# Optimization experiments

Measured on AMD Instinct MI355X. Metric: run time of the kernel, lower is better.

The kernel has to match this reference:

```python
import jax, jax.numpy as jnp
import numpy as np

B, N, T, D, DG, DS, NC = 16, 64, 256, 64, 64, 9, 2

def _pe(times, d, max_len):
    # PositionalEncodingTF: timescales = max_len ** linspace(0,1,d//2)
    ts = jnp.asarray(max_len ** np.linspace(0.0, 1.0, d // 2), jnp.float32)
    st = times[..., None] / ts
    return jnp.concatenate([jnp.sin(st), jnp.cos(st)], -1)

def _ln(h, g, b):
    m = h.mean(-1, keepdims=True)
    v = ((h - m) ** 2).mean(-1, keepdims=True)
    return (h - m) * jax.lax.rsqrt(v + 1e-5) * g + b

def setup_inputs():
    key = jax.random.key(0)
    ks = jax.random.split(key, 40)
    s = 0.02
    value = jax.random.normal(ks[0], (B, T, N))
    obs = (jax.random.uniform(ks[1], (B, T, N)) < 0.5).astype(jnp.float32)
    times = jnp.sort(jax.random.uniform(ks[2], (B, T)) * T, axis=1)
    F = D + 2 * DG  # per-node GRU input feature size [x_t, h, time_enc]
    return dict(
        x=jnp.concatenate([value, obs, times[..., None]], -1),
        nufft=jax.random.normal(ks[3], (B, 2, T, N)),
        delta_t=jax.random.uniform(ks[4], (B, T)) * 0.1,
        static=jax.random.normal(ks[5], (B, DS)),
        lengths=jax.random.randint(ks[6], (B,), 1, T + 1),
        proj_w=jax.random.normal(ks[7], (2, D)) * s, proj_b=jnp.zeros(D),
        Wqkv=jax.random.normal(ks[8], (D, 3 * D)) * s, bqkv=jnp.zeros(3 * D),
        Wo=jax.random.normal(ks[9], (D, D)) * s, bo=jnp.zeros(D),
        ln1_g=jnp.ones(D), ln1_b=jnp.zeros(D),
        W1=jax.random.normal(ks[10], (D, D)) * s, b1=jnp.zeros(D),
        W2=jax.random.normal(ks[11], (D, D)) * s, b2=jnp.zeros(D),
        ln2_g=jnp.ones(D), ln2_b=jnp.zeros(D),
        WQ_f=jax.random.normal(ks[12], (T, T)) * 0.05,
        WK_f=jax.random.normal(ks[13], (T, T)) * 0.05,
        Wz=jax.random.normal(ks[14], (2 * F, DG)) * s, bz=jnp.zeros(DG),
        Wr=jax.random.normal(ks[15], (2 * F, DG)) * s, br=jnp.zeros(DG),
        Wc=jax.random.normal(ks[16], (2 * F, DG)) * s, bc=jnp.zeros(DG),
        Wfin=jax.random.normal(ks[17], (DG,)) * s, bfin=jnp.zeros(()),
        We=jax.random.normal(ks[18], (DS, N)) * s, be=jnp.zeros(N),
        Wc1=jax.random.normal(ks[19], (2 * N, 200)) * s, bc1=jnp.zeros(200),
        Wc2=jax.random.normal(ks[20], (200, NC)) * s, bc2=jnp.zeros(NC),
    )

def _forward(x, nufft, delta_t, static, lengths, proj_w, proj_b, Wqkv, bqkv, Wo, bo,
             ln1_g, ln1_b, W1, b1, W2, b2, ln2_g, ln2_b, WQ_f, WK_f,
             Wz, bz, Wr, br, Wc, bc, Wfin, bfin, We, be, Wc1, bc1, Wc2, bc2):
    lengths = jnp.maximum(lengths, 1)
    value = x[:, :, :N].transpose(0, 2, 1)          # (B,N,T)
    obs = x[:, :, N:2 * N].transpose(0, 2, 1)       # (B,N,T) observation mask
    times = x[:, :, -1]                              # (B,T)
    # Conv2d(2->D, 1x1) input projection == per-element linear over [value, mask]
    feat = jnp.stack([value, obs], -1) @ proj_w + proj_b   # (B,N,T,D)
    pe1 = _pe(times, D, T)                           # (B,T,D)
    tin = feat + pe1[:, None]                        # (B,N,T,D)
    # single-head transformer encoder layer (post-norm, relu FFN, eval: no dropout)
    qkv = tin @ Wqkv + bqkv
    q, k, v = jnp.split(qkv, 3, -1)
    scores = jnp.einsum('bnqd,bnkd->bnqk', q, k) / jnp.sqrt(jnp.float32(D))
    kpad = jnp.arange(T)[None, :] >= lengths[:, None]      # (B,T) key padding
    scores = jnp.where(kpad[:, None, None, :], -1e9, scores)
    attn = jax.nn.softmax(scores, -1)
    ao = jnp.einsum('bnqk,bnkd->bnqd', attn, v) @ Wo + bo
    h1 = _ln(tin + ao, ln1_g, ln1_b)
    ff = jax.nn.relu(h1 @ W1 + b1) @ W2 + b2
    tout = _ln(h1 + ff, ln2_g, ln2_b)
    m = obs[..., None]
    x_tat = m * tin + (1.0 - m) * tout               # masked blend (B,N,T,D)
    # Variable_Attention_layer on nufft channel 1: relu-score softmax attention
    xf = nufft[:, 1].transpose(0, 2, 1)              # (B,N,T)
    S = jax.nn.relu(jnp.einsum('bnt,bmt->bnm', xf @ WQ_f, xf @ WK_f)) / jnp.sqrt(jnp.float32(T))
    A = jax.nn.softmax(S, -1).mean(0)                # (N,N)
    A = 0.5 * (A + A.T)
    sm = jax.nn.softmax(A, -1)
    A = 0.5 * (sm + sm.T)
    pe2 = _pe(times, DG, T)                          # (B,T,DG)
    # graph-conv GRU over time (CGRNN) with delta_t decay + length masking
    def stepf(h, inputs):
        xt, tet, dtt, t = inputs                     # (B,N,D),(B,DG),(B,),()
        h = h * jnp.exp(-jax.nn.relu(dtt))[:, None, None]
        te = jnp.broadcast_to(tet[:, None, :], (h.shape[0], N, DG))
        inp = jnp.concatenate([xt, h, te], -1)
        gin = jnp.concatenate([inp, jnp.einsum('nm,bmf->bnf', A, inp)], -1)
        z = jax.nn.sigmoid(gin @ Wz + bz)
        r = jax.nn.sigmoid(gin @ Wr + br)
        inc = jnp.concatenate([xt, r * h, te], -1)
        cin = jnp.concatenate([inc, jnp.einsum('nm,bmf->bnf', A, inc)], -1)
        c = jnp.tanh(cin @ Wc + bc)
        hn = z * h + (1.0 - z) * c
        h = jnp.where((t < lengths)[:, None, None], hn, h)
        return h, None
    h0 = jnp.zeros((x.shape[0], N, DG), x.dtype)
    xs = (x_tat.transpose(2, 0, 1, 3), pe2.transpose(1, 0, 2), delta_t.T, jnp.arange(T))
    hT, _ = jax.lax.scan(stepf, h0, xs)
    out = hT @ Wfin + bfin                           # final 1x1 conv -> (B,N)
    emb = static @ We + be                           # (B,N)
    hcl = jax.nn.relu(jnp.concatenate([out, emb], -1) @ Wc1 + bc1)
    return hcl @ Wc2 + bc2                           # (B,NC)

def reference(x, nufft, delta_t, static, lengths, proj_w, proj_b, Wqkv, bqkv, Wo, bo,
              ln1_g, ln1_b, W1, b1, W2, b2, ln2_g, ln2_b, WQ_f, WK_f,
              Wz, bz, Wr, br, Wc, bc, Wfin, bfin, We, be, Wc1, bc1, Wc2, bc2):
    return _forward(x, nufft, delta_t, static, lengths, proj_w, proj_b, Wqkv, bqkv, Wo, bo,
                    ln1_g, ln1_b, W1, b1, W2, b2, ln2_g, ln2_b, WQ_f, WK_f,
                    Wz, bz, Wr, br, Wc, bc, Wfin, bfin, We, be, Wc1, bc1, Wc2, bc2)
```

## Files before the change

### kernel.cpp

```cpp
#include <hip/hip_runtime.h>
#include <hip/hip_bf16.h>
#include <cmath>

#define DEV __device__ __forceinline__

typedef short s16x8 __attribute__((ext_vector_type(8)));
typedef short s16x4 __attribute__((ext_vector_type(4)));
typedef float f32x4 __attribute__((ext_vector_type(4)));
typedef int   i32x2 __attribute__((ext_vector_type(2)));

DEV unsigned short f2bu(float x){
  __hip_bfloat16 h = __float2bfloat16(x);
  return *reinterpret_cast<unsigned short*>(&h);
}
DEV float bs2f(unsigned short v){ return __uint_as_float(((unsigned)v)<<16); }
DEV float bs2f(short v){ return bs2f((unsigned short)v); }

DEV unsigned cvtpk(float lo, float hi){
  unsigned r;
  asm("v_cvt_pk_bf16_f32 %0, %1, %2" : "=v"(r) : "v"(lo), "v"(hi));
  return r;
}
DEV float dppx1(float v){
  int r = __builtin_amdgcn_mov_dpp(__float_as_int(v), 0xB1, 0xF, 0xF, true);
  return __int_as_float(r);
}

#define BAR() do { asm volatile("s_waitcnt lgkmcnt(0)" ::: "memory"); \
                   __builtin_amdgcn_s_barrier(); \
                   __builtin_amdgcn_sched_barrier(0); } while(0)

DEV int swzo(int row, int col){
  return (row*128 + ((col*2) ^ ((row&7)<<4))) >> 1;
}
DEV s16x8 ldfrag(const short* tile, int t16, int lane, int kk){
  int row = t16 + (lane & 15);
  int c0  = (kk<<5) + ((lane>>4)<<3);
  int off = (row*128 + ((c0<<1) ^ ((row&7)<<4))) >> 1;
  return *(const s16x8*)(tile + off);
}
DEV int swzv(int d, int t){
  return (d*512 + ((t*2) ^ ((d&7)<<4))) >> 1;
}

__global__ void k0_prep(const float* __restrict__ Wqkv, const float* __restrict__ Wo,
                        const float* __restrict__ W1, const float* __restrict__ W2,
                        const float* __restrict__ Wz, const float* __restrict__ Wr,
                        const float* __restrict__ Wc,
                        short* __restrict__ Wqkv_t, short* __restrict__ Wo_t,
                        short* __restrict__ W1_t, short* __restrict__ W2_t,
                        short* __restrict__ Wg_t, short* __restrict__ Wg_h)
{
  int t = blockIdx.x*256 + threadIdx.x;
  if (t < 12288){ int nn=t>>6, k=t&63; Wqkv_t[t]=(short)f2bu(Wqkv[k*192+nn]); }
  else if (t < 16384){ int e=t-12288; int nn=e>>6,k=e&63; Wo_t[e]=(short)f2bu(Wo[k*64+nn]); }
  else if (t < 20480){ int e=t-16384; int nn=e>>6,k=e&63; W1_t[e]=(short)f2bu(W1[k*64+nn]); }
  else if (t < 24576){ int e=t-20480; int nn=e>>6,k=e&63; W2_t[e]=(short)f2bu(W2[k*64+nn]); }
  else if (t < 49152){
    int e=t-24576;
    int g=e>>13, rem=e&8191, s=rem>>12, rem2=rem&4095, c=rem2>>6, k=rem2&63;
    const float* Wg = (g==0)?Wz:((g==1)?Wr:Wc);
    Wg_t[e] = (short)f2bu(Wg[((s?192:0)+k)*64 + c]);
  }
  else if (t < 73728){
    int e=t-49152;
    int g=e>>13, rem=e&8191, s=rem>>12, rem2=rem&4095, c=rem2>>6, k=rem2&63;
    const float* Wg = (g==0)?Wz:((g==1)?Wr:Wc);
    Wg_h[e] = (short)f2bu(Wg[((s?256:64)+k)*64 + c]);
  }
}

__global__ void k1_pe_u(const float* __restrict__ x, const float* __restrict__ delta_t,
                        const float* __restrict__ Wz, const float* __restrict__ bz,
                        const float* __restrict__ Wr, const float* __restrict__ br,
                        const float* __restrict__ Wc, const float* __restrict__ bc,
                        float* __restrict__ pe, float* __restrict__ U, float* __restrict__ decay)
{
  const int bt = blockIdx.x;
  const int d  = threadIdx.x;
  __shared__ float pes[64];
  float tmv = x[(size_t)bt*129 + 128];
  int j = d & 31;
  float ts = exp2f((float)j * (8.0f/31.0f));
  float st = tmv / ts;
  float v = (d < 32) ? sinf(st) : cosf(st);
  pes[d] = v;
  pe[(size_t)bt*64 + d] = v;
  __syncthreads();
  float a0=bz[d], a1=0.f, a2=br[d], a3=0.f, a4=bc[d], a5=0.f;
  for (int k=0;k<64;k++){
    float p = pes[k];
    a0 = fmaf(p, Wz[(128+k)*64+d], a0);
    a1 = fmaf(p, Wz[(320+k)*64+d], a1);
    a2 = fmaf(p, Wr[(128+k)*64+d], a2);
    a3 = fmaf(p, Wr[(320+k)*64+d], a3);
    a4 = fmaf(p, Wc[(128+k)*64+d], a4);
    a5 = fmaf(p, Wc[(320+k)*64+d], a5);
  }
  float* u = U + (size_t)bt*384;
  u[d]=a0; u[64+d]=a1; u[128+d]=a2; u[192+d]=a3; u[256+d]=a4; u[320+d]=a5;
  if (d==0) decay[bt] = expf(-fmaxf(delta_t[bt], 0.f));
}

__global__ void k2a_qfkf(const float* __restrict__ nufft, const float* __restrict__ WQf,
                         const float* __restrict__ WKf, float* __restrict__ qf, float* __restrict__ kf)
{
  const int bn = blockIdx.x, b = bn>>6, n = bn&63;
  const int u = threadIdx.x;
  __shared__ float xs[256];
  xs[u] = nufft[ ((((size_t)b*2)+1)*256 + u)*64 + n ];
  __syncthreads();
  float aq=0.f, ak=0.f;
  for (int t=0;t<256;t++){
    float xv = xs[t];
    aq = fmaf(xv, WQf[t*256+u], aq);
    ak = fmaf(xv, WKf[t*256+u], ak);
  }
  qf[(size_t)bn*256+u]=aq;
  kf[(size_t)bn*256+u]=ak;
}

__launch_bounds__(256, 1)
__global__ void k2b_soft(const float* __restrict__ qf, const float* __restrict__ kf,
                         float* __restrict__ soft)
{
  const int b = blockIdx.x, tid = threadIdx.x;
  __shared__ float qs[64*257];
  __shared__ float ksh[64*257];
  __shared__ float Ss[64*65];
  const float* qb = qf + ((size_t)b<<14);
  const float* kb = kf + ((size_t)b<<14);
  for (int e=tid; e<16384; e+=256){
    int r=e>>8, c=e&255;
    qs[r*257+c]=qb[e];
    ksh[r*257+c]=kb[e];
  }
  __syncthreads();
  const int n = tid>>2, m0 = (tid&3)<<4;
  float acc[16];
  #pragma unroll
  for (int i=0;i<16;i++) acc[i]=0.f;
  for (int t=0;t<256;t++){
    float qv = qs[n*257+t];
    #pragma unroll
    for (int i=0;i<16;i++) acc[i] = fmaf(qv, ksh[(m0+i)*257+t], acc[i]);
  }
  #pragma unroll
  for (int i=0;i<16;i++) Ss[n*65+m0+i] = fmaxf(acc[i],0.f)*(1.f/16.f);
  __syncthreads();
  if (tid < 64){
    float mx=-1e30f;
    for (int m=0;m<64;m++) mx=fmaxf(mx, Ss[tid*65+m]);
    float s=0.f;
    for (int m=0;m<64;m++) s += expf(Ss[tid*65+m]-mx);
    float inv=1.f/s;
    for (int m=0;m<64;m++) soft[((size_t)b<<12)+(tid<<6)+m] = expf(Ss[tid*65+m]-mx)*inv;
  }
}

__global__ void k2c_A(const float* __restrict__ soft, short* __restrict__ Abf,
                      float* __restrict__ rs_out)
{
  const int tid = threadIdx.x;
  __shared__ float A0[64*65];
  __shared__ float A1[64*65];
  for (int e=tid; e<4096; e+=256){
    int nn=e>>6, mm=e&63;
    float s=0.f;
    #pragma unroll
    for (int b=0;b<16;b++) s += soft[((size_t)b<<12)+e];
    A0[nn*65+mm] = s*(1.f/16.f);
  }
  __syncthreads();
  for (int e=tid; e<4096; e+=256){
    int nn=e>>6, mm=e&63;
    A1[nn*65+mm] = 0.5f*(A0[nn*65+mm]+A0[mm*65+nn]);
  }
  __syncthreads();
// ... 247 lines not shown
      const int rb=(rt<<4)+(lhi<<2);
      #pragma unroll
      for (int dt=0;dt<4;dt++){
        const int col=(dt<<4)+l15;
        const short* wb = W1_t + (col<<6)+(lhi<<3);
        s16x8 b0=*(const s16x8*)wb, b1v=*(const s16x8*)(wb+32);
        float bias=b1[col];
        f32x4 acc={bias,bias,bias,bias};
        acc=__builtin_amdgcn_mfma_f32_16x16x32_bf16(a0,b0,acc,0,0,0);
        acc=__builtin_amdgcn_mfma_f32_16x16x32_bf16(a1,b1v,acc,0,0,0);
        #pragma unroll
        for(int i=0;i<4;i++) tp_s[swzo(rb+i,col)]=(short)f2bu(fmaxf(acc[i],0.f));
      }
    }
  }
  __syncthreads();

  #pragma unroll
  for (int j=0;j<2;j++){
    const int rt=w+(j<<3);
    if (rt < LT){
      s16x8 a0=ldfrag(tp_s, rt<<4, lane, 0);
      s16x8 a1=ldfrag(tp_s, rt<<4, lane, 1);
      const int rb=(rt<<4)+(lhi<<2);
      f32x4 to[4];
      #pragma unroll
      for (int dt=0;dt<4;dt++){
        const int col=(dt<<4)+l15;
        const short* wb = W2_t + (col<<6)+(lhi<<3);
        s16x8 b0=*(const s16x8*)wb, b1v=*(const s16x8*)(wb+32);
        float bias=b2[col];
        f32x4 acc={bias,bias,bias,bias};
        acc=__builtin_amdgcn_mfma_f32_16x16x32_bf16(a0,b0,acc,0,0,0);
        acc=__builtin_amdgcn_mfma_f32_16x16x32_bf16(a1,b1v,acc,0,0,0);
        acc += h1[j][dt];
        to[dt]=acc;
      }
      f32x4 mu, rsq;
      #pragma unroll
      for(int i=0;i<4;i++){
        float sv = to[0][i]+to[1][i]+to[2][i]+to[3][i];
        sv += __shfl_xor(sv,1); sv+=__shfl_xor(sv,2); sv+=__shfl_xor(sv,4); sv+=__shfl_xor(sv,8);
        mu[i]=sv*(1.f/64.f);
      }
      #pragma unroll
      for(int i=0;i<4;i++){
        float sv=0.f;
        #pragma unroll
        for(int dt=0;dt<4;dt++){ float c=to[dt][i]-mu[i]; sv=fmaf(c,c,sv); }
        sv += __shfl_xor(sv,1); sv+=__shfl_xor(sv,2); sv+=__shfl_xor(sv,4); sv+=__shfl_xor(sv,8);
        rsq[i]=1.f/sqrtf(sv*(1.f/64.f)+1e-5f);
      }
      #pragma unroll
      for(int dt=0;dt<4;dt++){
        const int col=(dt<<4)+l15;
        float g=ln2g[col], bb=ln2b[col];
        #pragma unroll
        for(int i=0;i<4;i++){
          const int row=rb+i;
          if (row < len){
            float tv=(to[dt][i]-mu[i])*rsq[i]*g+bb;
            float tin = fmaf(valr[row],proj_w[col], fmaf(obsr[row],proj_w[64+col], proj_b[col]))
                      + pe_g[(((size_t)b<<8)+row)*64+col];
            float ob = obsr[row];
            xtat[((size_t)bn<<14)+(row<<6)+col] = f2bu(ob*tin + (1.f-ob)*tv);
          }
        }
      }
    }
  }
}

__global__ void k35_xg(const unsigned short* __restrict__ xtat, const short* __restrict__ Abf,
                       const short* __restrict__ Wg_t, const int* __restrict__ lengths,
                       const float* __restrict__ U, const float* __restrict__ rs_g,
                       unsigned short* __restrict__ Xall)
{
  const int bt = blockIdx.x, b = bt>>8, t = bt&255;
  int len = lengths[b]; if (len<1) len=1;
  if (t >= len) return;
  const int tid = threadIdx.x, w = tid>>6, lane = tid&63;
  const int l15 = lane&15, lhi = lane>>4;
  __shared__ short xt_rm[4096], xt_tp[4096], axt_rm[4096];

  #pragma unroll
  for (int q=0;q<2;q++){
    int e = tid + (q<<8);
    int nn = e>>3, c0 = (e&7)<<3;
    s16x8 v = *(const s16x8*)((const short*)xtat + (((size_t)(b*64+nn)*256 + t)<<6) + c0);
    *(s16x8*)(xt_rm + swzo(nn,c0)) = v;
    #pragma unroll
    for (int jj=0;jj<8;jj++) xt_tp[swzo(c0+jj, nn)] = v[jj];
  }
  __syncthreads();

  {
    s16x8 bx[2];
    #pragma unroll
    for (int kk=0;kk<2;kk++) bx[kk]=ldfrag(xt_tp, w<<4, lane, kk);
    #pragma unroll
    for (int rt=0;rt<4;rt++){
      f32x4 acc={0.f,0.f,0.f,0.f};
      #pragma unroll
      for (int kk=0;kk<2;kk++){
        s16x8 af = *(const s16x8*)(Abf + ((rt<<4)+l15)*64 + (kk<<5) + (lhi<<3));
        acc=__builtin_amdgcn_mfma_f32_16x16x32_bf16(af,bx[kk],acc,0,0,0);
      }
      const int rb=(rt<<4)+(lhi<<2);
      #pragma unroll
      for(int i=0;i<4;i++) axt_rm[swzo(rb+i,(w<<4)+l15)] = (short)f2bu(acc[i]);
    }
  }
  __syncthreads();

  s16x8 fx[4][2], fa[4][2];
  #pragma unroll
  for (int rt=0;rt<4;rt++)
    #pragma unroll
    for (int kk=0;kk<2;kk++){
      fx[rt][kk]=ldfrag(xt_rm, rt<<4, lane, kk);
      fa[rt][kk]=ldfrag(axt_rm, rt<<4, lane, kk);
    }
  const int dcol = (w<<4)+l15;
  f32x4 rsv[4];
  #pragma unroll
  for (int rt=0;rt<4;rt++) rsv[rt] = *(const f32x4*)(rs_g + (rt<<4) + (lhi<<2));
  const float* Ub = U + (size_t)bt*384;
  #pragma unroll
  for (int g=0; g<3; g++){
    s16x8 wbx[2], wba[2];
    #pragma unroll
    for (int kk=0;kk<2;kk++){
      wbx[kk] = *(const s16x8*)(Wg_t + (((g<<1)  )*64 + dcol)*64 + (kk<<5)+(lhi<<3));
      wba[kk] = *(const s16x8*)(Wg_t + (((g<<1)+1)*64 + dcol)*64 + (kk<<5)+(lhi<<3));
    }
    float u1 = Ub[(g<<7) + dcol];
    float u2 = Ub[(g<<7) + 64 + dcol];
    #pragma unroll
    for (int rt=0;rt<4;rt++){
      f32x4 acc={u1,u1,u1,u1};
      #pragma unroll
      for (int kk=0;kk<2;kk++){
        acc=__builtin_amdgcn_mfma_f32_16x16x32_bf16(fx[rt][kk],wbx[kk],acc,0,0,0);
        acc=__builtin_amdgcn_mfma_f32_16x16x32_bf16(fa[rt][kk],wba[kk],acc,0,0,0);
      }
      s16x4 pk;
      #pragma unroll
      for(int i=0;i<4;i++) pk[i]=(short)f2bu(acc[i] + rsv[rt][i]*u2);
      *(s16x4*)((short*)Xall + (((size_t)bt*3 + g)*64 + dcol)*64 + (rt<<4)+(lhi<<2)) = pk;
    }
  }
}

__launch_bounds__(512, 1)
__global__ void k4_scan(const unsigned short* __restrict__ Xall,
                        const float* __restrict__ decay, const short* __restrict__ Abf,
                        const short* __restrict__ Wg_h,
                        const int* __restrict__ lengths, float* __restrict__ hT)
{
  const int b = blockIdx.x, tid = threadIdx.x;
  const int w = tid>>6, lane = tid&63;
  const int l15 = lane&15, lhi = lane>>4;
  const int pe_ = l15&1;
  const int rnt = w>>1, dp = w&1;
  const int nb_ = (rnt<<4) + (lhi<<2);
  const int d0 = (dp<<5) + l15, d1 = (dp<<5) + 16 + l15;
  const int tmA0 = (w&1)<<1, tmA1 = tmA0+1;
  const int dnA = w>>1;

  __shared__ short h_rm[4096], h_tp[4096], ah_rm[4096];
  __shared__ short rh_rm[4096], rh_tp[4096], arh_rm[4096];
  __shared__ float dec_s[256];

  int len = lengths[b]; if (len<1) len=1;
  for (int e=tid; e<256; e+=512) dec_s[e] = decay[b*256+e];

  s16x8 aA[2][2];
  #pragma unroll
  for (int t2=0;t2<2;t2++)
    #pragma unroll
    for (int kk=0;kk<2;kk++)
      aA[t2][kk] = *(const s16x8*)(Abf + (((t2?tmA1:tmA0)<<4) + l15)*64 + (kk<<5) + (lhi<<3));

  s16x8 wf[3][2][2][2];
  #pragma unroll
  for (int g=0;g<3;g++)
    #pragma unroll
    for (int s=0;s<2;s++)
      #pragma unroll
      for (int kk=0;kk<2;kk++)
        #pragma unroll
        for (int e=0;e<2;e++)
          wf[g][s][kk][e] = *(const s16x8*)(Wg_h + (((g*2+s)*64 + (e?d1:d0))<<6) + (kk<<5) + (lhi<<3));

  int tpo[2];
  #pragma unroll
  for (int e=0;e<2;e++){ int r = e?d1:d0; tpo[e] = r*128 + (((nb_)*2) ^ ((r&7)<<4)); }
  int rmo[4];
  { int dPr = ((dp<<1) + pe_)*16 + (l15 & ~1);
    #pragma unroll
    for (int i=0;i<4;i++){ int n = nb_+i; rmo[i] = n*128 + ((dPr*2) ^ ((n&7)<<4)); } }
  int amo[4];
  { int dAr = (dnA<<4) + (l15 & ~1);
    int tb = (pe_? tmA1 : tmA0)<<4;
    #pragma unroll
    for (int i=0;i<4;i++){ int n = tb + (lhi<<2) + i; amo[i] = n*128 + ((dAr*2) ^ ((n&7)<<4)); } }
  int rdT[2], rdR[2];
  { int r = (dnA<<4)+l15;
    #pragma unroll
    for (int kk=0;kk<2;kk++) rdT[kk] = r*128 + (((kk<<6) + (lhi<<4)) ^ ((r&7)<<4)); }
  { int r = (rnt<<4)+l15;
    #pragma unroll
    for (int kk=0;kk<2;kk++) rdR[kk] = r*128 + (((kk<<6) + (lhi<<4)) ^ ((r&7)<<4)); }

  f32x4 hreg[2] = {{0.f,0.f,0.f,0.f},{0.f,0.f,0.f,0.f}};
  f32x4 zz[2];

  const short* Xb = (const short*)Xall;
  s16x4 xzc[2], xrc[2], xcc[2], xzn[2], xrn[2], xcn[2];
  #pragma unroll
  for (int e=0;e<2;e++){ xzc[e]=(s16x4){0,0,0,0}; xrc[e]=xzc[e]; xcc[e]=xzc[e]; }
  {
    const short* base = Xb + ((size_t)(b*256))*12288;
    #pragma unroll
    for (int e=0;e<2;e++){
      int de = e?d1:d0;
      xzc[e] = *(const s16x4*)(base + (0*64 + de)*64 + nb_);
      xrc[e] = *(const s16x4*)(base + (1*64 + de)*64 + nb_);
      xcc[e] = *(const s16x4*)(base + (2*64 + de)*64 + nb_);
    }
  }
  __syncthreads();

  for (int t=0; t<len; t++){
    float dc = dec_s[t];
    #pragma unroll
    for (int e=0;e<2;e++)
      #pragma unroll
      for (int i=0;i<4;i++) hreg[e][i] *= dc;

    #pragma unroll
    for (int e=0;e<2;e++){ xzn[e]=(s16x4){0,0,0,0}; xrn[e]=xzn[e]; xcn[e]=xzn[e]; }
    if (t+1 < len){
      const short* base = Xb + ((size_t)(b*256 + t+1))*12288;
      #pragma unroll
      for (int e=0;e<2;e++){
        int de = e?d1:d0;
        xzn[e] = *(const s16x4*)(base + (0*64 + de)*64 + nb_);
        xrn[e] = *(const s16x4*)(base + (1*64 + de)*64 + nb_);
        xcn[e] = *(const s16x4*)(base + (2*64 + de)*64 + nb_);
      }
    }

    #pragma unroll
    for (int e=0;e<2;e++){
      i32x2 v; v[0] = (int)cvtpk(hreg[e][0], hreg[e][1]);
               v[1] = (int)cvtpk(hreg[e][2], hreg[e][3]);
      *(i32x2*)((char*)h_tp + tpo[e]) = v;
    }
    #pragma unroll
    for (int i=0;i<4;i++){
      float v0 = hreg[0][i], v1 = hreg[1][i];
      float n0 = dppx1(v0), n1 = dppx1(v1);
      float lo = pe_ ? n1 : v0;
      float hi = pe_ ? v1 : n0;
      *(unsigned*)((char*)h_rm + rmo[i]) = cvtpk(lo, hi);
    }
    BAR();

    {
      s16x8 bh0 = *(const s16x8*)((const char*)h_tp + rdT[0]);
      s16x8 bh1 = *(const s16x8*)((const char*)h_tp + rdT[1]);
      f32x4 a0v={0.f,0.f,0.f,0.f}, a1v={0.f,0.f,0.f,0.f};
      a0v = __builtin_amdgcn_mfma_f32_16x16x32_bf16(aA[0][0], bh0, a0v, 0,0,0);
      a0v = __builtin_amdgcn_mfma_f32_16x16x32_bf16(aA[0][1], bh1, a0v, 0,0,0);
      a1v = __builtin_amdgcn_mfma_f32_16x16x32_bf16(aA[1][0], bh0, a1v, 0,0,0);
      a1v = __builtin_amdgcn_mfma_f32_16x16x32_bf16(aA[1][1], bh1, a1v, 0,0,0);
      #pragma unroll
      for (int i=0;i<4;i++){
        float n0 = dppx1(a0v[i]), n1 = dppx1(a1v[i]);
        float lo = pe_ ? n1 : a0v[i];
        float hi = pe_ ? a1v[i] : n0;
        *(unsigned*)((char*)ah_rm + amo[i]) = cvtpk(lo, hi);
      }
    }
    BAR();

    {
      s16x8 fh0 = *(const s16x8*)((const char*)h_rm  + rdR[0]);
      s16x8 fh1 = *(const s16x8*)((const char*)h_rm  + rdR[1]);
      s16x8 fa0 = *(const s16x8*)((const char*)ah_rm + rdR[0]);
      s16x8 fa1 = *(const s16x8*)((const char*)ah_rm + rdR[1]);
      f32x4 gz[2], gr[2], rh[2];
      #pragma unroll
      for (int e=0;e<2;e++)
        #pragma unroll
        for (int i=0;i<4;i++){ gz[e][i]=bs2f(xzc[e][i]); gr[e][i]=bs2f(xrc[e][i]); }
      #pragma unroll
      for (int e=0;e<2;e++){
        gz[e] = __builtin_amdgcn_mfma_f32_16x16x32_bf16(fh0, wf[0][0][0][e], gz[e], 0,0,0);
        gz[e] = __builtin_amdgcn_mfma_f32_16x16x32_bf16(fh1, wf[0][0][1][e], gz[e], 0,0,0);
        gz[e] = __builtin_amdgcn_mfma_f32_16x16x32_bf16(fa0, wf[0][1][0][e], gz[e], 0,0,0);
        gz[e] = __builtin_amdgcn_mfma_f32_16x16x32_bf16(fa1, wf[0][1][1][e], gz[e], 0,0,0);
        gr[e] = __builtin_amdgcn_mfma_f32_16x16x32_bf16(fh0, wf[1][0][0][e], gr[e], 0,0,0);
        gr[e] = __builtin_amdgcn_mfma_f32_16x16x32_bf16(fh1, wf[1][0][1][e], gr[e], 0,0,0);
        gr[e] = __builtin_amdgcn_mfma_f32_16x16x32_bf16(fa0, wf[1][1][0][e], gr[e], 0,0,0);
        gr[e] = __builtin_amdgcn_mfma_f32_16x16x32_bf16(fa1, wf[1][1][1][e], gr[e], 0,0,0);
      }
      #pragma unroll
      for (int e=0;e<2;e++)
        #pragma unroll
        for (int i=0;i<4;i++){
          float zv = 1.f/(1.f+__expf(-gz[e][i]));
          float rv = 1.f/(1.f+__expf(-gr[e][i]));
          zz[e][i] = zv;
          rh[e][i] = rv * hreg[e][i];
        }
      #pragma unroll
      for (int e=0;e<2;e++){
        i32x2 v; v[0] = (int)cvtpk(rh[e][0], rh[e][1]);
                 v[1] = (int)cvtpk(rh[e][2], rh[e][3]);
        *(i32x2*)((char*)rh_tp + tpo[e]) = v;
      }
      #pragma unroll
      for (int i=0;i<4;i++){
        float v0 = rh[0][i], v1 = rh[1][i];
        float n0 = dppx1(v0), n1 = dppx1(v1);
        float lo = pe_ ? n1 : v0;
        float hi = pe_ ? v1 : n0;
        *(unsigned*)((char*)rh_rm + rmo[i]) = cvtpk(lo, hi);
      }
    }
    BAR();

    {
      s16x8 br0 = *(const s16x8*)((const char*)rh_tp + rdT[0]);
      s16x8 br1 = *(const s16x8*)((const char*)rh_tp + rdT[1]);
      f32x4 a0v={0.f,0.f,0.f,0.f}, a1v={0.f,0.f,0.f,0.f};
      a0v = __builtin_amdgcn_mfma_f32_16x16x32_bf16(aA[0][0], br0, a0v, 0,0,0);
      a0v = __builtin_amdgcn_mfma_f32_16x16x32_bf16(aA[0][1], br1, a0v, 0,0,0);
      a1v = __builtin_amdgcn_mfma_f32_16x16x32_bf16(aA[1][0], br0, a1v, 0,0,0);
      a1v = __builtin_amdgcn_mfma_f32_16x16x32_bf16(aA[1][1], br1, a1v, 0,0,0);
      #pragma unroll
      for (int i=0;i<4;i++){
        float n0 = dppx1(a0v[i]), n1 = dppx1(a1v[i]);
        float lo = pe_ ? n1 : a0v[i];
        float hi = pe_ ? a1v[i] : n0;
        *(unsigned*)((char*)arh_rm + amo[i]) = cvtpk(lo, hi);
      }
    }
    BAR();

    {
      s16x8 fr0 = *(const s16x8*)((const char*)rh_rm  + rdR[0]);
      s16x8 fr1 = *(const s16x8*)((const char*)rh_rm  + rdR[1]);
      s16x8 fb0 = *(const s16x8*)((const char*)arh_rm + rdR[0]);
      s16x8 fb1 = *(const s16x8*)((const char*)arh_rm + rdR[1]);
      f32x4 gc[2];
      #pragma unroll
      for (int e=0;e<2;e++)
        #pragma unroll
        for (int i=0;i<4;i++) gc[e][i]=bs2f(xcc[e][i]);
      #pragma unroll
      for (int e=0;e<2;e++){
        gc[e] = __builtin_amdgcn_mfma_f32_16x16x32_bf16(fr0, wf[2][0][0][e], gc[e], 0,0,0);
        gc[e] = __builtin_amdgcn_mfma_f32_16x16x32_bf16(fr1, wf[2][0][1][e], gc[e], 0,0,0);
        gc[e] = __builtin_amdgcn_mfma_f32_16x16x32_bf16(fb0, wf[2][1][0][e], gc[e], 0,0,0);
        gc[e] = __builtin_amdgcn_mfma_f32_16x16x32_bf16(fb1, wf[2][1][1][e], gc[e], 0,0,0);
      }
      #pragma unroll
      for (int e=0;e<2;e++)
        #pragma unroll
        for (int i=0;i<4;i++){
          float cv = 1.f - 2.f/(__expf(2.f*gc[e][i])+1.f);
          hreg[e][i] = fmaf(zz[e][i], hreg[e][i]-cv, cv);
        }
    }

    #pragma unroll
    for (int e=0;e<2;e++){ xzc[e]=xzn[e]; xrc[e]=xrn[e]; xcc[e]=xcn[e]; }
  }

  float sp = 1.f;
  for (int t=len; t<256; t++) sp *= dec_s[t];
  #pragma unroll
  for (int e=0;e<2;e++)
    #pragma unroll
    for (int i=0;i<4;i++)
      hT[(((size_t)b<<6) + nb_ + i)*64 + (e?d1:d0)] = hreg[e][i]*sp;
}

__global__ void k5_head(const float* __restrict__ hT, const float* __restrict__ Wfin,
                        const float* __restrict__ bfin,
                        const float* __restrict__ stat, const float* __restrict__ We,
                        const float* __restrict__ be,
                        const float* __restrict__ Wc1, const float* __restrict__ bc1,
                        const float* __restrict__ Wc2, const float* __restrict__ bc2,
                        float* __restrict__ out)
{
  const int b = blockIdx.x, tid = threadIdx.x;
  __shared__ float cat[128];
  __shared__ float hcl[200];
  if (tid < 64){
    const float* hr = hT + (((size_t)b<<6)+tid)*64;
    float a = bfin[0];
    #pragma unroll
    for (int d=0;d<64;d++) a = fmaf(hr[d], Wfin[d], a);
    cat[tid]=a;
  } else if (tid < 128){
    int nn = tid-64;
    float a = be[nn];
    #pragma unroll
    for (int k=0;k<9;k++) a = fmaf(stat[b*9+k], We[k*64+nn], a);
    cat[tid]=a;
  }
  __syncthreads();
  if (tid < 200){
    float a = bc1[tid];
    for (int k=0;k<128;k++) a = fmaf(cat[k], Wc1[k*200+tid], a);
    hcl[tid] = fmaxf(a, 0.f);
  }
  __syncthreads();
  if (tid < 2){
    float a = bc2[tid];
    for (int k=0;k<200;k++) a = fmaf(hcl[k], Wc2[k*2+tid], a);
    out[b*2+tid] = a;
  }
}

extern "C" void kernel_launch(void* const* d_in, const int* in_sizes, int n_in,
                              void* d_out, int out_size, void* d_ws, size_t ws_size,
                              hipStream_t stream)
{
  const float* x       = (const float*)d_in[0];
  const float* nufft   = (const float*)d_in[1];
  const float* delta_t = (const float*)d_in[2];
  const float* stat    = (const float*)d_in[3];
  const int*   lengths = (const int*)  d_in[4];
  const float* proj_w  = (const float*)d_in[5];
  const float* proj_b  = (const float*)d_in[6];
  const float* Wqkv    = (const float*)d_in[7];
  const float* bqkv    = (const float*)d_in[8];
  const float* Wo      = (const float*)d_in[9];
  const float* bo      = (const float*)d_in[10];
  const float* ln1g    = (const float*)d_in[11];
  const float* ln1b    = (const float*)d_in[12];
  const float* W1      = (const float*)d_in[13];
  const float* b1      = (const float*)d_in[14];
  const float* W2      = (const float*)d_in[15];
  const float* b2      = (const float*)d_in[16];
  const float* ln2g    = (const float*)d_in[17];
  const float* ln2b    = (const float*)d_in[18];
  const float* WQf     = (const float*)d_in[19];
  const float* WKf     = (const float*)d_in[20];
  const float* Wz      = (const float*)d_in[21];
  const float* bz      = (const float*)d_in[22];
  const float* Wr      = (const float*)d_in[23];
  const float* br      = (const float*)d_in[24];
  const float* Wc      = (const float*)d_in[25];
  const float* bc      = (const float*)d_in[26];
  const float* Wfin    = (const float*)d_in[27];
  const float* bfin    = (const float*)d_in[28];
  const float* We      = (const float*)d_in[29];
  const float* be      = (const float*)d_in[30];
  const float* Wc1     = (const float*)d_in[31];
  const float* bc1     = (const float*)d_in[32];
  const float* Wc2     = (const float*)d_in[33];
  const float* bc2     = (const float*)d_in[34];
  float* out = (float*)d_out;

  char* ws = (char*)d_ws;
  size_t o = 0;
  float* pe    = (float*)(ws+o); o += (size_t)4096*64*4;
  float* U     = (float*)(ws+o); o += (size_t)4096*384*4;
  float* decay = (float*)(ws+o); o += (size_t)4096*4;
  unsigned short* xtat = (unsigned short*)(ws+o); o += (size_t)1024*256*64*2;
  float* qf    = (float*)(ws+o); o += (size_t)1024*256*4;
  float* kf    = (float*)(ws+o); o += (size_t)1024*256*4;
  float* soft  = (float*)(ws+o); o += (size_t)16*4096*4;
  short* Abf   = (short*)(ws+o); o += (size_t)4096*2;
  float* rs    = (float*)(ws+o); o += (size_t)64*4;
  float* hT    = (float*)(ws+o); o += (size_t)16*64*64*4;
  short* Wqkv_t= (short*)(ws+o); o += (size_t)12288*2;
  short* Wo_t  = (short*)(ws+o); o += (size_t)4096*2;
  short* W1_t  = (short*)(ws+o); o += (size_t)4096*2;
  short* W2_t  = (short*)(ws+o); o += (size_t)4096*2;
  short* Wg_t  = (short*)(ws+o); o += (size_t)24576*2;
  short* Wg_h  = (short*)(ws+o); o += (size_t)24576*2;
  unsigned short* Xall = (unsigned short*)(ws+o); o += (size_t)4096*3*4096*2;
  (void)ws_size; (void)in_sizes; (void)n_in; (void)out_size;

  hipLaunchKernelGGL(k0_prep,   dim3(288),  dim3(256), 0, stream,
                     Wqkv, Wo, W1, W2, Wz, Wr, Wc, Wqkv_t, Wo_t, W1_t, W2_t, Wg_t, Wg_h);
  hipLaunchKernelGGL(k1_pe_u,   dim3(4096), dim3(64),  0, stream,
                     x, delta_t, Wz, bz, Wr, br, Wc, bc, pe, U, decay);
  hipLaunchKernelGGL(k2a_qfkf,  dim3(1024), dim3(256), 0, stream,
                     nufft, WQf, WKf, qf, kf);
  hipLaunchKernelGGL(k2b_soft,  dim3(16),   dim3(256), 0, stream, qf, kf, soft);
  hipLaunchKernelGGL(k2c_A,     dim3(1),    dim3(256), 0, stream, soft, Abf, rs);
  hipLaunchKernelGGL(k3_former, dim3(1024), dim3(512), 0, stream,
                     x, pe, proj_w, proj_b, Wqkv_t, bqkv, Wo_t, bo, ln1g, ln1b,
                     W1_t, b1, W2_t, b2, ln2g, ln2b, lengths, xtat);
  hipLaunchKernelGGL(k35_xg,    dim3(4096), dim3(256), 0, stream,
                     xtat, Abf, Wg_t, lengths, U, rs, Xall);
  hipLaunchKernelGGL(k4_scan,   dim3(16),   dim3(512), 0, stream,
                     Xall, decay, Abf, Wg_h, lengths, hT);
  hipLaunchKernelGGL(k5_head,   dim3(16),   dim3(256), 0, stream,
                     hT, Wfin, bfin, stat, We, be, Wc1, bc1, Wc2, bc2, out);
}
```

Baseline: 864.9 us.

## Reassociate graph mixing after weight projection in GRU scan, cut barriers to two

The recurrent scan now computes (h·W_a) first and then applies the adjacency A to that product (A·(hW) instead of (A·h)·W). Each wave owns 16 output features for all 64 nodes, so the separate A·h and A·(r*h) stages and their shared-memory buffers go away. Each timestep now needs two barriers instead of four. The block shrinks from 512 to 256 threads, and the decay multiply moves to the end of the step. In exchange, each wave does more MFMA work per step, the intermediate is rounded to bf16 at a different point, and register pressure is higher.

```diff
diff --git a/kernel.cpp b/kernel.cpp
--- a/kernel.cpp
+++ b/kernel.cpp
@@ -24,6 +24,16 @@
 DEV float dppx1(float v){
   int r = __builtin_amdgcn_mov_dpp(__float_as_int(v), 0xB1, 0xF, 0xF, true);
   return __int_as_float(r);
+}
+DEV f32x4 mfma16(s16x4 a, s16x4 b, f32x4 c){
+  asm("v_mfma_f32_16x16x16_bf16 %0, %1, %2, %0" : "+v"(c) : "v"(a), "v"(b));
+  return c;
+}
+DEV s16x4 packbf(f32x4 v){
+  union { i32x2 u; s16x4 s; } r;
+  r.u[0] = (int)cvtpk(v[0], v[1]);
+  r.u[1] = (int)cvtpk(v[2], v[3]);
+  return r.s;
 }
 
 #define BAR() do { asm volatile("s_waitcnt lgkmcnt(0)" ::: "memory"); \
@@ -577,7 +587,7 @@
   }
 }
 
-__launch_bounds__(512, 1)
+__launch_bounds__(256, 1)
 __global__ void k4_scan(const unsigned short* __restrict__ Xall,
                         const float* __restrict__ decay, const short* __restrict__ Abf,
                         const short* __restrict__ Wg_h,
@@ -585,234 +595,221 @@
 {
   const int b = blockIdx.x, tid = threadIdx.x;
   const int w = tid>>6, lane = tid&63;
-  const int l15 = lane&15, lhi = lane>>4;
-  const int pe_ = l15&1;
-  const int rnt = w>>1, dp = w&1;
-  const int nb_ = (rnt<<4) + (lhi<<2);
-  const int d0 = (dp<<5) + l15, d1 = (dp<<5) + 16 + l15;
-  const int tmA0 = (w&1)<<1, tmA1 = tmA0+1;
-  const int dnA = w>>1;
-
-  __shared__ short h_rm[4096], h_tp[4096], ah_rm[4096];
-  __shared__ short rh_rm[4096], rh_tp[4096], arh_rm[4096];
+  const int l15 = lane&15, g = lane>>4;
+  const int pe = l15&1;
+  const int dg = (w<<4) + l15;
+
+  __shared__ short h_rm[4096];
+  __shared__ short rh_rm[4096];
   __shared__ float dec_s[256];
 
   int len = lengths[b]; if (len<1) len=1;
-  for (int e=tid; e<256; e+=512) dec_s[e] = decay[b*256+e];
-
-  s16x8 aA[2][2];
-  #pragma unroll
-  for (int t2=0;t2<2;t2++)
-    #pragma unroll
-    for (int kk=0;kk<2;kk++)
-      aA[t2][kk] = *(const s16x8*)(Abf + (((t2?tmA1:tmA0)<<4) + l15)*64 + (kk<<5) + (lhi<<3));
-
-  s16x8 wf[3][2][2][2];
-  #pragma unroll
-  for (int g=0;g<3;g++)
+  dec_s[tid] = decay[b*256+tid];
+
+  s16x4 aA[4][4];
+  #pragma unroll
+  for (int nt=0;nt<4;nt++)
+    #pragma unroll
+    for (int kc=0;kc<4;kc++)
+      aA[nt][kc] = *(const s16x4*)(Abf + ((nt<<4)+l15)*64 + (kc<<4) + (g<<2));
+
+  s16x8 wfB[3][2][2];
+  #pragma unroll
+  for (int g3=0;g3<3;g3++)
     #pragma unroll
     for (int s=0;s<2;s++)
       #pragma unroll
-      for (int kk=0;kk<2;kk++)
-        #pragma unroll
-        for (int e=0;e<2;e++)
-          wf[g][s][kk][e] = *(const s16x8*)(Wg_h + (((g*2+s)*64 + (e?d1:d0))<<6) + (kk<<5) + (lhi<<3));
-
-  int tpo[2];
-  #pragma unroll
-  for (int e=0;e<2;e++){ int r = e?d1:d0; tpo[e] = r*128 + (((nb_)*2) ^ ((r&7)<<4)); }
-  int rmo[4];
-  { int dPr = ((dp<<1) + pe_)*16 + (l15 & ~1);
-    #pragma unroll
-    for (int i=0;i<4;i++){ int n = nb_+i; rmo[i] = n*128 + ((dPr*2) ^ ((n&7)<<4)); } }
-  int amo[4];
-  { int dAr = (dnA<<4) + (l15 & ~1);
-    int tb = (pe_? tmA1 : tmA0)<<4;
-    #pragma unroll
-    for (int i=0;i<4;i++){ int n = tb + (lhi<<2) + i; amo[i] = n*128 + ((dAr*2) ^ ((n&7)<<4)); } }
-  int rdT[2], rdR[2];
-  { int r = (dnA<<4)+l15;
-    #pragma unroll
-    for (int kk=0;kk<2;kk++) rdT[kk] = r*128 + (((kk<<6) + (lhi<<4)) ^ ((r&7)<<4)); }
-  { int r = (rnt<<4)+l15;
-    #pragma unroll
-    for (int kk=0;kk<2;kk++) rdR[kk] = r*128 + (((kk<<6) + (lhi<<4)) ^ ((r&7)<<4)); }
-
-  f32x4 hreg[2] = {{0.f,0.f,0.f,0.f},{0.f,0.f,0.f,0.f}};
-  f32x4 zz[2];
-
-  const short* Xb = (const short*)Xall;
-  s16x4 xzc[2], xrc[2], xcc[2], xzn[2], xrn[2], xcn[2];
-  #pragma unroll
-  for (int e=0;e<2;e++){ xzc[e]=(s16x4){0,0,0,0}; xrc[e]=xzc[e]; xcc[e]=xzc[e]; }
+      for (int kc=0;kc<2;kc++)
+        wfB[g3][s][kc] = *(const s16x8*)(Wg_h + (((g3*2+s)*64 + dg)<<6) + (kc<<5) + (g<<3));
+
   {
-    const short* base = Xb + ((size_t)(b*256))*12288;
-    #pragma unroll
-    for (int e=0;e<2;e++){
-      int de = e?d1:d0;
-      xzc[e] = *(const s16x4*)(base + (0*64 + de)*64 + nb_);
-      xrc[e] = *(const s16x4*)(base + (1*64 + de)*64 + nb_);
-      xcc[e] = *(const s16x4*)(base + (2*64 + de)*64 + nb_);
-    }
-  }
+    s16x8 z8 = {0,0,0,0,0,0,0,0};
+    *(s16x8*)(h_rm + tid*16) = z8;
+    *(s16x8*)(h_rm + tid*16 + 8) = z8;
+  }
+
+  int rdo[4][2];
+  #pragma unroll
+  for (int nt=0;nt<4;nt++)
+    #pragma unroll
+    for (int kc=0;kc<2;kc++){
+      int r = (nt<<4) + l15;
+      rdo[nt][kc] = r*128 + (((kc<<6) + (g<<4)) ^ ((r&7)<<4));
+    }
+  int wro[4][2];
+  {
+    int pb = (w<<5) + ((l15&~1)<<1);
+    #pragma unroll
+    for (int nt=0;nt<4;nt++)
+      #pragma unroll
+      for (int q=0;q<2;q++){
+        int i = (pe<<1) + q;
+        int nrow = (nt<<4) + (g<<2) + i;
+        wro[nt][q] = nrow*128 + (pb ^ ((nrow&7)<<4));
+      }
+  }
+
+  f32x4 hreg[4] = {{0,0,0,0},{0,0,0,0},{0,0,0,0},{0,0,0,0}};
+  f32x4 zz[4];
+
+  const unsigned short* Xbase = Xall + ((size_t)(b*256))*12288;
+  int xoff[3][4];
+  #pragma unroll
+  for (int g3=0;g3<3;g3++)
+    #pragma unroll
+    for (int nt=0;nt<4;nt++)
+      xoff[g3][nt] = ((g3<<6) + dg)*64 + (nt<<4) + (g<<2);
+
+  s16x4 xc[3][4], xn[3][4];
+  #pragma unroll
+  for (int g3=0;g3<3;g3++)
+    #pragma unroll
+    for (int nt=0;nt<4;nt++)
+      xc[g3][nt] = *(const s16x4*)(Xbase + xoff[g3][nt]);
+
   __syncthreads();
 
   for (int t=0; t<len; t++){
-    float dc = dec_s[t];
-    #pragma unroll
-    for (int e=0;e<2;e++)
-      #pragma unroll
-      for (int i=0;i<4;i++) hreg[e][i] *= dc;
-
-    #pragma unroll
-    for (int e=0;e<2;e++){ xzn[e]=(s16x4){0,0,0,0}; xrn[e]=xzn[e]; xcn[e]=xzn[e]; }
     if (t+1 < len){
-      const short* base = Xb + ((size_t)(b*256 + t+1))*12288;
-      #pragma unroll
-      for (int e=0;e<2;e++){
-        int de = e?d1:d0;
-        xzn[e] = *(const s16x4*)(base + (0*64 + de)*64 + nb_);
-        xrn[e] = *(const s16x4*)(base + (1*64 + de)*64 + nb_);
-        xcn[e] = *(const s16x4*)(base + (2*64 + de)*64 + nb_);
-      }
-    }
-
-    #pragma unroll
-    for (int e=0;e<2;e++){
-      i32x2 v; v[0] = (int)cvtpk(hreg[e][0], hreg[e][1]);
-               v[1] = (int)cvtpk(hreg[e][2], hreg[e][3]);
-      *(i32x2*)((char*)h_tp + tpo[e]) = v;
-    }
+      const unsigned short* bp = Xbase + (size_t)(t+1)*12288;
+      #pragma unroll
+      for (int g3=0;g3<3;g3++)
+        #pragma unroll
+        for (int nt=0;nt<4;nt++)
+          xn[g3][nt] = *(const s16x4*)(bp + xoff[g3][nt]);
+    } else {
+      #pragma unroll
+      for (int g3=0;g3<3;g3++)
+        #pragma unroll
+        for (int nt=0;nt<4;nt++)
+          xn[g3][nt] = (s16x4){0,0,0,0};
+    }
+
+    s16x8 hf[4][2];
+    #pragma unroll
+    for (int nt=0;nt<4;nt++)
+      #pragma unroll
+      for (int kc=0;kc<2;kc++)
+        hf[nt][kc] = *(const s16x8*)((const char*)h_rm + rdo[nt][kc]);
+
+    f32x4 gz[4], gr[4], yz[4], yr[4];
+    #pragma unroll
+    for (int nt=0;nt<4;nt++){
+      #pragma unroll
+      for (int i=0;i<4;i++){
+        gz[nt][i] = bs2f(xc[0][nt][i]);
+        gr[nt][i] = bs2f(xc[1][nt][i]);
+      }
+      yz[nt] = (f32x4){0,0,0,0};
+      yr[nt] = (f32x4){0,0,0,0};
+    }
+    #pragma unroll
+    for (int nt=0;nt<4;nt++)
+      #pragma unroll
+      for (int kc=0;kc<2;kc++){
+        gz[nt] = __builtin_amdgcn_mfma_f32_16x16x32_bf16(hf[nt][kc], wfB[0][0][kc], gz[nt], 0,0,0);
+        yz[nt] = __builtin_amdgcn_mfma_f32_16x16x32_bf16(hf[nt][kc], wfB[0][1][kc], yz[nt], 0,0,0);
+        gr[nt] = __builtin_amdgcn_mfma_f32_16x16x32_bf16(hf[nt][kc], wfB[1][0][kc], gr[nt], 0,0,0);
+        yr[nt] = __builtin_amdgcn_mfma_f32_16x16x32_bf16(hf[nt][kc], wfB[1][1][kc], yr[nt], 0,0,0);
+      }
+    s16x4 yzp[4], yrp[4];
+    #pragma unroll
+    for (int nt=0;nt<4;nt++){ yzp[nt]=packbf(yz[nt]); yrp[nt]=packbf(yr[nt]); }
+    #pragma unroll
+    for (int nt=0;nt<4;nt++)
+      #pragma unroll
+      for (int kc=0;kc<4;kc++){
+        gz[nt] = mfma16(aA[nt][kc], yzp[kc], gz[nt]);
+        gr[nt] = mfma16(aA[nt][kc], yrp[kc], gr[nt]);
+      }
+    f32x4 rh[4];
+    #pragma unroll
+    for (int nt=0;nt<4;nt++)
+      #pragma unroll
+      for (int i=0;i<4;i++){
+        float zv = __builtin_amdgcn_rcpf(1.f + __expf(-gz[nt][i]));
+        float rv = __builtin_amdgcn_rcpf(1.f + __expf(-gr[nt][i]));
+        zz[nt][i] = zv;
+        rh[nt][i] = rv * hreg[nt][i];
+      }
+    #pragma unroll
+    for (int nt=0;nt<4;nt++)
+      #pragma unroll
+      for (int q=0;q<2;q++){
+        int i = (pe<<1) + q;
+        float v = rh[nt][i];
+        float nv = dppx1(v);
+        unsigned word = pe ? cvtpk(nv, v) : cvtpk(v, nv);
+        *(unsigned*)((char*)rh_rm + wro[nt][q]) = word;
+      }
+    BAR();
+
+    s16x8 rf[4][2];
+    #pragma unroll
+    for (int nt=0;nt<4;nt++)
+      #pragma unroll
+      for (int kc=0;kc<2;kc++)
+        rf[nt][kc] = *(const s16x8*)((const char*)rh_rm + rdo[nt][kc]);
+
+    f32x4 gc[4], yc[4];
+    #pragma unroll
+    for (int nt=0;nt<4;nt++){
+      #pragma unroll
+      for (int i=0;i<4;i++) gc[nt][i] = bs2f(xc[2][nt][i]);
+      yc[nt] = (f32x4){0,0,0,0};
+    }
+    #pragma unroll
+    for (int nt=0;nt<4;nt++)
+      #pragma unroll
+      for (int kc=0;kc<2;kc++){
+        gc[nt] = __builtin_amdgcn_mfma_f32_16x16x32_bf16(rf[nt][kc], wfB[2][0][kc], gc[nt], 0,0,0);
+        yc[nt] = __builtin_amdgcn_mfma_f32_16x16x32_bf16(rf[nt][kc], wfB[2][1][kc], yc[nt], 0,0,0);
+      }
+    s16x4 ycp[4];
+    #pragma unroll
+    for (int nt=0;nt<4;nt++) ycp[nt]=packbf(yc[nt]);
+    #pragma unroll
+    for (int nt=0;nt<4;nt++)
+      #pragma unroll
+      for (int kc=0;kc<4;kc++)
+        gc[nt] = mfma16(aA[nt][kc], ycp[kc], gc[nt]);
+
+    float dcn = (t+1 < len) ? dec_s[t+1] : 1.f;
+    #pragma unroll
+    for (int nt=0;nt<4;nt++)
+      #pragma unroll
+      for (int i=0;i<4;i++){
+        float cv = 1.f - 2.f*__builtin_amdgcn_rcpf(__expf(2.f*gc[nt][i]) + 1.f);
+        float hn = cv + zz[nt][i]*(hreg[nt][i] - cv);
+        hreg[nt][i] = hn * dcn;
+      }
+    #pragma unroll
+    for (int nt=0;nt<4;nt++)
+      #pragma unroll
+      for (int q=0;q<2;q++){
+        int i = (pe<<1) + q;
+        float v = hreg[nt][i];
+        float nv = dppx1(v);
+        unsigned word = pe ? cvtpk(nv, v) : cvtpk(v, nv);
+        *(unsigned*)((char*)h_rm + wro[nt][q]) = word;
+      }
+    #pragma unroll
+    for (int g3=0;g3<3;g3++)
+      #pragma unroll
+      for (int nt=0;nt<4;nt++)
+        xc[g3][nt] = xn[g3][nt];
+    BAR();
+  }
+
+  float sp = 1.f;
+  for (int t2=len; t2<256; t2++) sp *= dec_s[t2];
+  #pragma unroll
+  for (int nt=0;nt<4;nt++)
     #pragma unroll
     for (int i=0;i<4;i++){
-      float v0 = hreg[0][i], v1 = hreg[1][i];
-      float n0 = dppx1(v0), n1 = dppx1(v1);
-      float lo = pe_ ? n1 : v0;
-      float hi = pe_ ? v1 : n0;
-      *(unsigned*)((char*)h_rm + rmo[i]) = cvtpk(lo, hi);
-    }
-    BAR();
-
-    {
-      s16x8 bh0 = *(const s16x8*)((const char*)h_tp + rdT[0]);
-      s16x8 bh1 = *(const s16x8*)((const char*)h_tp + rdT[1]);
-      f32x4 a0v={0.f,0.f,0.f,0.f}, a1v={0.f,0.f,0.f,0.f};
-      a0v = __builtin_amdgcn_mfma_f32_16x16x32_bf16(aA[0][0], bh0, a0v, 0,0,0);
-      a0v = __builtin_amdgcn_mfma_f32_16x16x32_bf16(aA[0][1], bh1, a0v, 0,0,0);
-      a1v = __builtin_amdgcn_mfma_f32_16x16x32_bf16(aA[1][0], bh0, a1v, 0,0,0);
-      a1v = __builtin_amdgcn_mfma_f32_16x16x32_bf16(aA[1][1], bh1, a1v, 0,0,0);
-      #pragma unroll
-      for (int i=0;i<4;i++){
-        float n0 = dppx1(a0v[i]), n1 = dppx1(a1v[i]);
-        float lo = pe_ ? n1 : a0v[i];
-        float hi = pe_ ? a1v[i] : n0;
-        *(unsigned*)((char*)ah_rm + amo[i]) = cvtpk(lo, hi);
-      }
-    }
-    BAR();
-
-    {
-      s16x8 fh0 = *(const s16x8*)((const char*)h_rm  + rdR[0]);
-      s16x8 fh1 = *(const s16x8*)((const char*)h_rm  + rdR[1]);
-      s16x8 fa0 = *(const s16x8*)((const char*)ah_rm + rdR[0]);
-      s16x8 fa1 = *(const s16x8*)((const char*)ah_rm + rdR[1]);
-      f32x4 gz[2], gr[2], rh[2];
-      #pragma unroll
-      for (int e=0;e<2;e++)
-        #pragma unroll
-        for (int i=0;i<4;i++){ gz[e][i]=bs2f(xzc[e][i]); gr[e][i]=bs2f(xrc[e][i]); }
-      #pragma unroll
-      for (int e=0;e<2;e++){
-        gz[e] = __builtin_amdgcn_mfma_f32_16x16x32_bf16(fh0, wf[0][0][0][e], gz[e], 0,0,0);
-        gz[e] = __builtin_amdgcn_mfma_f32_16x16x32_bf16(fh1, wf[0][0][1][e], gz[e], 0,0,0);
-        gz[e] = __builtin_amdgcn_mfma_f32_16x16x32_bf16(fa0, wf[0][1][0][e], gz[e], 0,0,0);
-        gz[e] = __builtin_amdgcn_mfma_f32_16x16x32_bf16(fa1, wf[0][1][1][e], gz[e], 0,0,0);
-        gr[e] = __builtin_amdgcn_mfma_f32_16x16x32_bf16(fh0, wf[1][0][0][e], gr[e], 0,0,0);
-        gr[e] = __builtin_amdgcn_mfma_f32_16x16x32_bf16(fh1, wf[1][0][1][e], gr[e], 0,0,0);
-        gr[e] = __builtin_amdgcn_mfma_f32_16x16x32_bf16(fa0, wf[1][1][0][e], gr[e], 0,0,0);
-        gr[e] = __builtin_amdgcn_mfma_f32_16x16x32_bf16(fa1, wf[1][1][1][e], gr[e], 0,0,0);
-      }
-      #pragma unroll
-      for (int e=0;e<2;e++)
-        #pragma unroll
-        for (int i=0;i<4;i++){
-          float zv = 1.f/(1.f+__expf(-gz[e][i]));
-          float rv = 1.f/(1.f+__expf(-gr[e][i]));
-          zz[e][i] = zv;
-          rh[e][i] = rv * hreg[e][i];
-        }
-      #pragma unroll
-      for (int e=0;e<2;e++){
-        i32x2 v; v[0] = (int)cvtpk(rh[e][0], rh[e][1]);
-                 v[1] = (int)cvtpk(rh[e][2], rh[e][3]);
-        *(i32x2*)((char*)rh_tp + tpo[e]) = v;
-      }
-      #pragma unroll
-      for (int i=0;i<4;i++){
-        float v0 = rh[0][i], v1 = rh[1][i];
-        float n0 = dppx1(v0), n1 = dppx1(v1);
-        float lo = pe_ ? n1 : v0;
-        float hi = pe_ ? v1 : n0;
-        *(unsigned*)((char*)rh_rm + rmo[i]) = cvtpk(lo, hi);
-      }
-    }
-    BAR();
-
-    {
-      s16x8 br0 = *(const s16x8*)((const char*)rh_tp + rdT[0]);
-      s16x8 br1 = *(const s16x8*)((const char*)rh_tp + rdT[1]);
-      f32x4 a0v={0.f,0.f,0.f,0.f}, a1v={0.f,0.f,0.f,0.f};
-      a0v = __builtin_amdgcn_mfma_f32_16x16x32_bf16(aA[0][0], br0, a0v, 0,0,0);
-      a0v = __builtin_amdgcn_mfma_f32_16x16x32_bf16(aA[0][1], br1, a0v, 0,0,0);
-      a1v = __builtin_amdgcn_mfma_f32_16x16x32_bf16(aA[1][0], br0, a1v, 0,0,0);
-      a1v = __builtin_amdgcn_mfma_f32_16x16x32_bf16(aA[1][1], br1, a1v, 0,0,0);
-      #pragma unroll
-      for (int i=0;i<4;i++){
-        float n0 = dppx1(a0v[i]), n1 = dppx1(a1v[i]);
-        float lo = pe_ ? n1 : a0v[i];
-        float hi = pe_ ? a1v[i] : n0;
-        *(unsigned*)((char*)arh_rm + amo[i]) = cvtpk(lo, hi);
-      }
-    }
-    BAR();
-
-    {
-      s16x8 fr0 = *(const s16x8*)((const char*)rh_rm  + rdR[0]);
-      s16x8 fr1 = *(const s16x8*)((const char*)rh_rm  + rdR[1]);
-      s16x8 fb0 = *(const s16x8*)((const char*)arh_rm + rdR[0]);
-      s16x8 fb1 = *(const s16x8*)((const char*)arh_rm + rdR[1]);
-      f32x4 gc[2];
-      #pragma unroll
-      for (int e=0;e<2;e++)
-        #pragma unroll
-        for (int i=0;i<4;i++) gc[e][i]=bs2f(xcc[e][i]);
-      #pragma unroll
-      for (int e=0;e<2;e++){
-        gc[e] = __builtin_amdgcn_mfma_f32_16x16x32_bf16(fr0, wf[2][0][0][e], gc[e], 0,0,0);
-        gc[e] = __builtin_amdgcn_mfma_f32_16x16x32_bf16(fr1, wf[2][0][1][e], gc[e], 0,0,0);
-        gc[e] = __builtin_amdgcn_mfma_f32_16x16x32_bf16(fb0, wf[2][1][0][e], gc[e], 0,0,0);
-        gc[e] = __builtin_amdgcn_mfma_f32_16x16x32_bf16(fb1, wf[2][1][1][e], gc[e], 0,0,0);
-      }
-      #pragma unroll
-      for (int e=0;e<2;e++)
-        #pragma unroll
-        for (int i=0;i<4;i++){
-          float cv = 1.f - 2.f/(__expf(2.f*gc[e][i])+1.f);
-          hreg[e][i] = fmaf(zz[e][i], hreg[e][i]-cv, cv);
-        }
-    }
-
-    #pragma unroll
-    for (int e=0;e<2;e++){ xzc[e]=xzn[e]; xrc[e]=xrn[e]; xcc[e]=xcn[e]; }
-  }
-
-  float sp = 1.f;
-  for (int t=len; t<256; t++) sp *= dec_s[t];
-  #pragma unroll
-  for (int e=0;e<2;e++)
-    #pragma unroll
-    for (int i=0;i<4;i++)
-      hT[(((size_t)b<<6) + nb_ + i)*64 + (e?d1:d0)] = hreg[e][i]*sp;
+      int nrow = (nt<<4) + (g<<2) + i;
+      hT[(((size_t)b<<6) + nrow)*64 + dg] = hreg[nt][i]*sp;
+    }
 }
 
 __global__ void k5_head(const float* __restrict__ hT, const float* __restrict__ Wfin,
@@ -928,7 +925,7 @@
                      W1_t, b1, W2_t, b2, ln2g, ln2b, lengths, xtat);
   hipLaunchKernelGGL(k35_xg,    dim3(4096), dim3(256), 0, stream,
                      xtat, Abf, Wg_t, lengths, U, rs, Xall);
-  hipLaunchKernelGGL(k4_scan,   dim3(16),   dim3(512), 0, stream,
+  hipLaunchKernelGGL(k4_scan,   dim3(16),   dim3(256), 0, stream,
                      Xall, decay, Abf, Wg_h, lengths, hT);
   hipLaunchKernelGGL(k5_head,   dim3(16),   dim3(256), 0, stream,
                      hT, Wfin, bfin, stat, We, be, Wc1, bc1, Wc2, bc2, out);
```

Result: slower. 1.066 ms (+23.3%).
